# Performance work log

Hardware: AMD Instinct MI355X
Metric: run time of the kernel (lower is better)

Reference implementation:

```python
import jax, jax.numpy as jnp
import numpy as np

B, T, D, L = 16, 4096, 512, 1024

def setup_inputs() -> dict:
    key = jax.random.key(0)
    k1, k2, k3, k4 = jax.random.split(key, 4)
    x = jax.random.normal(k1, (B, T, D), dtype=jnp.float32)
    q = jax.random.normal(k2, (L, D), dtype=jnp.float32)
    fc_w = jax.random.normal(k3, (1, D), dtype=jnp.float32) * (1.0 / np.sqrt(D))
    fc_b = jax.random.normal(k4, (1,), dtype=jnp.float32) * 0.01
    return {"x": x, "q": q, "fc_w": fc_w, "fc_b": fc_b}

def reference(x, q, fc_w, fc_b):
    # att: (B, T, L) label-wise attention scores, softmax over sequence axis T
    att = jnp.einsum('btd,ld->btl', x, q)
    att = jax.nn.softmax(att, axis=1)
    # out: (B, L, D) attention-pooled features per label
    out = jnp.einsum('btl,btd->bld', att, x)
    # linear head to scalar per label -> (B, L)
    return jnp.einsum('bld,od->blo', out, fc_w).squeeze(-1) + fc_b[0]
```

## Files before the change

### kernel.cpp

```cpp
#include <hip/hip_runtime.h>

#define B_ 16
#define T_ 4096
#define D_ 512
#define L_ 1024
#define NTCH (T_ / 64)
#define PPLANE ((size_t)B_ * NTCH * L_)

typedef _Float16 half8 __attribute__((ext_vector_type(8)));
typedef float float4v __attribute__((ext_vector_type(4)));

__device__ inline void gl_lds(const void* g, void* l) {
    __builtin_amdgcn_global_load_lds(
        (const __attribute__((address_space(1))) unsigned int*)g,
        (__attribute__((address_space(3))) unsigned int*)l, 16, 0, 0);
}

__global__ __launch_bounds__(256) void k_prep(const float* __restrict__ src,
                                              const float* __restrict__ w,
                                              _Float16* __restrict__ dst,
                                              float* __restrict__ y, int do_y) {
    __shared__ float Yp[64];
    const int tid  = threadIdx.x;
    const int wv   = tid >> 6;
    const int lane = tid & 63;
    const int row  = lane & 15, gq = lane >> 4;
    const float* bsrc = src + (size_t)blockIdx.x * (16 * 512);
    half8* bdst = (half8*)dst + (size_t)blockIdx.x * 1024;

    float acc = 0.f;
#pragma unroll
    for (int it = 0; it < 4; ++it) {
        int kc = it * 4 + wv;
        int k0 = kc * 32 + gq * 8;
        float4 a = *(const float4*)(bsrc + row * 512 + k0);
        float4 c = *(const float4*)(bsrc + row * 512 + k0 + 4);
        half8 h;
        h[0] = (_Float16)a.x; h[1] = (_Float16)a.y; h[2] = (_Float16)a.z; h[3] = (_Float16)a.w;
        h[4] = (_Float16)c.x; h[5] = (_Float16)c.y; h[6] = (_Float16)c.z; h[7] = (_Float16)c.w;
        bdst[kc * 64 + lane] = h;
        if (do_y) {
            float4 wa = *(const float4*)(w + k0);
            float4 wc = *(const float4*)(w + k0 + 4);
            acc = fmaf(a.x, wa.x, acc); acc = fmaf(a.y, wa.y, acc);
            acc = fmaf(a.z, wa.z, acc); acc = fmaf(a.w, wa.w, acc);
            acc = fmaf(c.x, wc.x, acc); acc = fmaf(c.y, wc.y, acc);
            acc = fmaf(c.z, wc.z, acc); acc = fmaf(c.w, wc.w, acc);
        }
    }
    if (do_y) {
        acc += __shfl_xor(acc, 16, 64);
        acc += __shfl_xor(acc, 32, 64);
        if (gq == 0) Yp[wv * 16 + row] = acc;
        __syncthreads();
        if (tid < 16)
            y[blockIdx.x * 16 + tid] = Yp[tid] + Yp[16 + tid] + Yp[32 + tid] + Yp[48 + tid];
    }
}

__global__ __launch_bounds__(256, 4) void k_mfma(const _Float16* __restrict__ xt,
                                                 const _Float16* __restrict__ qt,
                                                 const float* __restrict__ y,
                                                 float* __restrict__ part) {
    __shared__ half8 S[1024];
    __shared__ float ys[128];

    const int bid  = blockIdx.x;
    const int xcd  = bid & 7;
    const int jj   = bid >> 3;
    const int tile = (xcd << 6) | (jj >> 3);
    const int lblk = jj & 7;
    const int tblk = tile & 31;
    const int b    = tile >> 5;

    const int tid  = threadIdx.x;
    const int lane = tid & 63;
    const int w    = tid >> 6;
    const int tb0  = b * (T_ / 16) + tblk * 8;
    const int lb0  = lblk * 8;

    if (tid < 128) ys[tid] = y[(size_t)b * T_ + tblk * 128 + tid];

    float4v acc[4][4];
#pragma unroll
    for (int i = 0; i < 4; ++i)
#pragma unroll
        for (int j = 0; j < 4; ++j) acc[i][j] = (float4v){0.f, 0.f, 0.f, 0.f};

    const half8* Xg = (const half8*)xt;
    const half8* Qg = (const half8*)qt;
    const int xa = tb0 + 2 * w;
    const int qa = lb0 + 2 * w;
    const int ts = (w >> 1) * 4, ls = (w & 1) * 4;

    for (int kc = 0; kc < D_ / 32; ++kc) {
        __syncthreads();
        gl_lds(Xg + ((size_t)xa * (D_ / 32) + kc) * 64 + lane,       &S[(2 * w) * 64]);
        gl_lds(Xg + ((size_t)(xa + 1) * (D_ / 32) + kc) * 64 + lane, &S[(2 * w + 1) * 64]);
        gl_lds(Qg + ((size_t)qa * (D_ / 32) + kc) * 64 + lane,       &S[512 + (2 * w) * 64]);
        gl_lds(Qg + ((size_t)(qa + 1) * (D_ / 32) + kc) * 64 + lane, &S[512 + (2 * w + 1) * 64]);
        __syncthreads();

        half8 A[4], Bv[4];
#pragma unroll
        for (int i = 0; i < 4; ++i) A[i] = S[(ts + i) * 64 + lane];
#pragma unroll
        for (int j = 0; j < 4; ++j) Bv[j] = S[512 + (ls + j) * 64 + lane];
#pragma unroll
        for (int i = 0; i < 4; ++i)
#pragma unroll
            for (int j = 0; j < 4; ++j)
                acc[i][j] = __builtin_amdgcn_mfma_f32_16x16x32_f16(A[i], Bv[j], acc[i][j], 0, 0, 0);
    }

    const int quad = lane >> 4, cl = lane & 15;
    const int tw = (w >> 1) * 64;
    const int tchunk = tblk * 2 + (w >> 1);
    const int lbase = lblk * 128 + (w & 1) * 64;

    float* pm = part;
    float* pz = part + PPLANE;
    float* pn = part + 2 * PPLANE;

#pragma unroll
    for (int j = 0; j < 4; ++j) {
        float m = -1e30f;
#pragma unroll
        for (int i = 0; i < 4; ++i)
#pragma unroll
            for (int r = 0; r < 4; ++r) m = fmaxf(m, acc[i][j][r]);
        float z = 0.f, n = 0.f;
#pragma unroll
        for (int i = 0; i < 4; ++i)
#pragma unroll
            for (int r = 0; r < 4; ++r) {
                float p = __expf(acc[i][j][r] - m);
                z += p;
                n = fmaf(p, ys[tw + i * 16 + quad * 4 + r], n);
            }
#pragma unroll
        for (int msk = 16; msk <= 32; msk <<= 1) {
            float om = __shfl_xor(m, msk, 64);
            float oz = __shfl_xor(z, msk, 64);
            float on = __shfl_xor(n, msk, 64);
            float mn = fmaxf(m, om);
            float s0 = __expf(m - mn), s1 = __expf(om - mn);
            z = fmaf(z, s0, oz * s1);
            n = fmaf(n, s0, on * s1);
            m = mn;
        }
        if (quad == 0) {
            int l = lbase + j * 16 + cl;
            size_t a = ((size_t)b * NTCH + tchunk) * L_ + l;
            pm[a] = m;
            pz[a] = z;
            pn[a] = n;
        }
    }
}

__global__ __launch_bounds__(256) void k_comb_p(const float* __restrict__ part,
                                                const float* __restrict__ fc_b,
                                                float* __restrict__ out) {
    int bl = blockIdx.x * 256 + threadIdx.x;
    int b = bl >> 10, l = bl & (L_ - 1);
    const float* pm = part;
    const float* pz = part + PPLANE;
    const float* pn = part + 2 * PPLANE;
    float m = -1e30f, z = 0.f, n = 0.f;
    for (int c = 0; c < NTCH; ++c) {
        size_t a = ((size_t)b * NTCH + c) * L_ + l;
        float pmv = pm[a], pzv = pz[a], pnv = pn[a];
        float mn = fmaxf(m, pmv);
        float s0 = __expf(m - mn), s1 = __expf(pmv - mn);
        z = fmaf(z, s0, pzv * s1);
        n = fmaf(n, s0, pnv * s1);
        m = mn;
    }
    out[bl] = n / z + fc_b[0];
}

#define NC 8
#define TC (T_ / NC)
#define BT 128
#define BL 128
#define KK 32

__global__ __launch_bounds__(256) void k_y(const float* __restrict__ x,
                                           const float* __restrict__ w,
                                           float* __restrict__ y) {
    int row  = (blockIdx.x * 256 + threadIdx.x) >> 6;
    int lane = threadIdx.x & 63;
    const float* r = x + (size_t)row * D_;
    float s = 0.f;
#pragma unroll
    for (int k = 0; k < D_; k += 64) s = fmaf(r[k + lane], w[k + lane], s);
#pragma unroll
    for (int o = 32; o > 0; o >>= 1) s += __shfl_xor(s, o, 64);
    if (lane == 0) y[row] = s;
}

__global__ __launch_bounds__(256, 2) void k_main(const float* __restrict__ x,
                                                 const float* __restrict__ q,
                                                 const float* __restrict__ y,
                                                 float* __restrict__ part) {
    __shared__ float Xs[KK][BT + 4];
    __shared__ float Qs[KK][BL + 4];
    const int tid = threadIdx.x;
    const int ty = tid & 15, tx = tid >> 4;
    const int lb = blockIdx.x * BL, chunk = blockIdx.y, b = blockIdx.z;
    const int g = tid & 7, r0 = tid >> 3;

    float run_m[8], run_z[8], run_n[8];
#pragma unroll
    for (int j = 0; j < 8; ++j) { run_m[j] = -1e30f; run_z[j] = 0.f; run_n[j] = 0.f; }

    for (int tt = 0; tt < TC; tt += BT) {
        const int t0 = chunk * TC + tt;
        float s[8][8];
#pragma unroll
        for (int i = 0; i < 8; ++i)
#pragma unroll
            for (int j = 0; j < 8; ++j) s[i][j] = 0.f;
        for (int kc = 0; kc < D_; kc += KK) {
            __syncthreads();
#pragma unroll
            for (int p = 0; p < 4; ++p) {
                int rr = p * 32 + r0;
                float4 vx = *(const float4*)(x + ((size_t)b * T_ + t0 + rr) * D_ + kc + g * 4);
                float4 vq = *(const float4*)(q + (size_t)(lb + rr) * D_ + kc + g * 4);
                Xs[g * 4 + 0][rr] = vx.x; Xs[g * 4 + 1][rr] = vx.y;
                Xs[g * 4 + 2][rr] = vx.z; Xs[g * 4 + 3][rr] = vx.w;
                Qs[g * 4 + 0][rr] = vq.x; Qs[g * 4 + 1][rr] = vq.y;
                Qs[g * 4 + 2][rr] = vq.z; Qs[g * 4 + 3][rr] = vq.w;
            }
            __syncthreads();
#pragma unroll
            for (int k = 0; k < KK; ++k) {
                float4 a0 = *(const float4*)&Xs[k][ty * 4];
                float4 a1 = *(const float4*)&Xs[k][64 + ty * 4];
                float4 b0 = *(const float4*)&Qs[k][tx * 4];
                float4 b1 = *(const float4*)&Qs[k][64 + tx * 4];
                float av[8] = {a0.x, a0.y, a0.z, a0.w, a1.x, a1.y, a1.z, a1.w};
                float bv[8] = {b0.x, b0.y, b0.z, b0.w, b1.x, b1.y, b1.z, b1.w};
#pragma unroll
                for (int i = 0; i < 8; ++i)
#pragma unroll
                    for (int j = 0; j < 8; ++j) s[i][j] = fmaf(av[i], bv[j], s[i][j]);
            }
        }
        float yv[8];
#pragma unroll
        for (int i = 0; i < 8; ++i) {
            int tl = (i < 4) ? (ty * 4 + i) : (64 + ty * 4 + (i - 4));
            yv[i] = y[(size_t)b * T_ + t0 + tl];
        }
#pragma unroll
        for (int j = 0; j < 8; ++j) {
            float mt = s[0][j];
#pragma unroll
            for (int i = 1; i < 8; ++i) mt = fmaxf(mt, s[i][j]);
            float mn = fmaxf(run_m[j], mt);
            float sc = __expf(run_m[j] - mn);
            float z = run_z[j] * sc, n = run_n[j] * sc;
#pragma unroll
            for (int i = 0; i < 8; ++i) {
                float p = __expf(s[i][j] - mn);
                z += p;
                n = fmaf(p, yv[i], n);
            }
            run_m[j] = mn; run_z[j] = z; run_n[j] = n;
        }
    }
#pragma unroll
    for (int msk = 1; msk < 16; msk <<= 1) {
#pragma unroll
        for (int j = 0; j < 8; ++j) {
            float om = __shfl_xor(run_m[j], msk, 64);
            float oz = __shfl_xor(run_z[j], msk, 64);
            float on = __shfl_xor(run_n[j], msk, 64);
            float mn = fmaxf(run_m[j], om);
            float s0 = __expf(run_m[j] - mn), s1 = __expf(om - mn);
            run_z[j] = fmaf(run_z[j], s0, oz * s1);
            run_n[j] = fmaf(run_n[j], s0, on * s1);
            run_m[j] = mn;
        }
    }
    if (ty == 0) {
#pragma unroll
        for (int j = 0; j < 8; ++j) {
            int ll = (j < 4) ? (tx * 4 + j) : (64 + tx * 4 + (j - 4));
            size_t idx = ((size_t)(b * L_ + lb + ll) * NC + chunk) * 3;
            part[idx + 0] = run_m[j];
            part[idx + 1] = run_z[j];
            part[idx + 2] = run_n[j];
        }
    }
}

__global__ __launch_bounds__(256) void k_comb_f(const float* __restrict__ part,
                                                const float* __restrict__ fc_b,
                                                float* __restrict__ out) {
    int bl = blockIdx.x * 256 + threadIdx.x;
    float m = -1e30f, z = 0.f, n = 0.f;
    for (int c = 0; c < NC; ++c) {
        size_t idx = ((size_t)bl * NC + c) * 3;
        float pm = part[idx + 0], pz = part[idx + 1], pn = part[idx + 2];
        float mn = fmaxf(m, pm);
        float s0 = __expf(m - mn), s1 = __expf(pm - mn);
        z = fmaf(z, s0, pz * s1);
        n = fmaf(n, s0, pn * s1);
        m = mn;
    }
    out[bl] = n / z + fc_b[0];
}

extern "C" void kernel_launch(void* const* d_in, const int* in_sizes, int n_in,
                              void* d_out, int out_size, void* d_ws, size_t ws_size,
                              hipStream_t stream) {
    const float* x    = (const float*)d_in[0];
    const float* q    = (const float*)d_in[1];
    const float* fc_w = (const float*)d_in[2];
    const float* fc_b = (const float*)d_in[3];
    float* out = (float*)d_out;
    float* ws  = (float*)d_ws;

    const size_t Y_F    = (size_t)B_ * T_;
    const size_t PART_F = 3 * PPLANE;
    const size_t XT_H   = (size_t)B_ * T_ * D_;
    const size_t QT_H   = (size_t)L_ * D_;
    const size_t need   = (Y_F + PART_F) * 4 + (XT_H + QT_H) * 2;

    if (ws_size >= need) {
        float* y    = ws;
        float* part = ws + Y_F;
        _Float16* xt = (_Float16*)(ws + Y_F + PART_F);
        _Float16* qt = xt + XT_H;
        k_prep<<<B_ * T_ / 16, 256, 0, stream>>>(x, fc_w, xt, y, 1);
        k_prep<<<L_ / 16, 256, 0, stream>>>(q, fc_w, qt, nullptr, 0);
        k_mfma<<<4096, 256, 0, stream>>>(xt, qt, y, part);
        k_comb_p<<<B_ * L_ / 256, 256, 0, stream>>>(part, fc_b, out);
    } else {
        float* y    = ws;
        float* part = ws + Y_F;
        k_y   <<<B_ * T_ / 4, 256, 0, stream>>>(x, fc_w, y);
        k_main<<<dim3(L_ / BL, NC, B_), 256, 0, stream>>>(x, q, y, part);
        k_comb_f<<<B_ * L_ / 256, 256, 0, stream>>>(part, fc_b, out);
    }
}
```

Baseline: 290.6 us.

## Stage prep rows through LDS, merge prep launches, double K-step per sync in MFMA

The prep kernel now loads each 16x512 fp32 tile with fully coalesced float4 reads into padded shared memory before converting to fp16. The separate x and q prep launches are merged into one grid, saving a launch. The MFMA kernel loads two 32-wide K chunks per barrier pair, halving the number of synchronisations at the cost of doubling LDS use per block to 32KB. That may lower occupancy at the requested 4 blocks per SM.

```diff
diff --git a/kernel.cpp b/kernel.cpp
--- a/kernel.cpp
+++ b/kernel.cpp
@@ -6,6 +6,7 @@
 #define L_ 1024
 #define NTCH (T_ / 64)
 #define PPLANE ((size_t)B_ * NTCH * L_)
+#define XBLK (B_ * T_ / 16)
 
 typedef _Float16 half8 __attribute__((ext_vector_type(8)));
 typedef float float4v __attribute__((ext_vector_type(4)));
@@ -16,30 +17,42 @@
         (__attribute__((address_space(3))) unsigned int*)l, 16, 0, 0);
 }
 
-__global__ __launch_bounds__(256) void k_prep(const float* __restrict__ src,
+__global__ __launch_bounds__(256) void k_prep(const float* __restrict__ x,
+                                              const float* __restrict__ q,
                                               const float* __restrict__ w,
-                                              _Float16* __restrict__ dst,
-                                              float* __restrict__ y, int do_y) {
+                                              _Float16* __restrict__ xt,
+                                              _Float16* __restrict__ qt,
+                                              float* __restrict__ y) {
+    __shared__ float Xl[16 * 516];
     __shared__ float Yp[64];
-    const int tid  = threadIdx.x;
-    const int wv   = tid >> 6;
-    const int lane = tid & 63;
-    const int row  = lane & 15, gq = lane >> 4;
-    const float* bsrc = src + (size_t)blockIdx.x * (16 * 512);
-    half8* bdst = (half8*)dst + (size_t)blockIdx.x * 1024;
-
+    const int tid = threadIdx.x;
+    const bool isq = blockIdx.x >= XBLK;
+    const int blk = isq ? (blockIdx.x - XBLK) : blockIdx.x;
+    const float* bsrc = (isq ? q : x) + (size_t)blk * (16 * 512);
+    half8* dst = (half8*)(isq ? qt : xt) + (size_t)blk * 1024;
+
+#pragma unroll
+    for (int it = 0; it < 8; ++it) {
+        int f = it * 1024 + tid * 4;
+        int row = f >> 9, k = f & 511;
+        *(float4*)&Xl[row * 516 + k] = *(const float4*)(bsrc + f);
+    }
+    __syncthreads();
+
+    const int wv = tid >> 6, lane = tid & 63;
+    const int row = lane & 15, gq = lane >> 4;
     float acc = 0.f;
 #pragma unroll
     for (int it = 0; it < 4; ++it) {
         int kc = it * 4 + wv;
         int k0 = kc * 32 + gq * 8;
-        float4 a = *(const float4*)(bsrc + row * 512 + k0);
-        float4 c = *(const float4*)(bsrc + row * 512 + k0 + 4);
+        float4 a = *(const float4*)&Xl[row * 516 + k0];
+        float4 c = *(const float4*)&Xl[row * 516 + k0 + 4];
         half8 h;
         h[0] = (_Float16)a.x; h[1] = (_Float16)a.y; h[2] = (_Float16)a.z; h[3] = (_Float16)a.w;
         h[4] = (_Float16)c.x; h[5] = (_Float16)c.y; h[6] = (_Float16)c.z; h[7] = (_Float16)c.w;
-        bdst[kc * 64 + lane] = h;
-        if (do_y) {
+        dst[kc * 64 + lane] = h;
+        if (!isq) {
             float4 wa = *(const float4*)(w + k0);
             float4 wc = *(const float4*)(w + k0 + 4);
             acc = fmaf(a.x, wa.x, acc); acc = fmaf(a.y, wa.y, acc);
@@ -48,13 +61,13 @@
             acc = fmaf(c.z, wc.z, acc); acc = fmaf(c.w, wc.w, acc);
         }
     }
-    if (do_y) {
+    if (!isq) {
         acc += __shfl_xor(acc, 16, 64);
         acc += __shfl_xor(acc, 32, 64);
         if (gq == 0) Yp[wv * 16 + row] = acc;
         __syncthreads();
         if (tid < 16)
-            y[blockIdx.x * 16 + tid] = Yp[tid] + Yp[16 + tid] + Yp[32 + tid] + Yp[48 + tid];
+            y[blk * 16 + tid] = Yp[tid] + Yp[16 + tid] + Yp[32 + tid] + Yp[48 + tid];
     }
 }
 
@@ -62,7 +75,7 @@
                                                  const _Float16* __restrict__ qt,
                                                  const float* __restrict__ y,
                                                  float* __restrict__ part) {
-    __shared__ half8 S[1024];
+    __shared__ half8 S[2048];
     __shared__ float ys[128];
 
     const int bid  = blockIdx.x;
@@ -93,24 +106,35 @@
     const int qa = lb0 + 2 * w;
     const int ts = (w >> 1) * 4, ls = (w & 1) * 4;
 
-    for (int kc = 0; kc < D_ / 32; ++kc) {
+    for (int kk = 0; kk < D_ / 64; ++kk) {
+        const int kc0 = kk * 2;
         __syncthreads();
-        gl_lds(Xg + ((size_t)xa * (D_ / 32) + kc) * 64 + lane,       &S[(2 * w) * 64]);
-        gl_lds(Xg + ((size_t)(xa + 1) * (D_ / 32) + kc) * 64 + lane, &S[(2 * w + 1) * 64]);
-        gl_lds(Qg + ((size_t)qa * (D_ / 32) + kc) * 64 + lane,       &S[512 + (2 * w) * 64]);
-        gl_lds(Qg + ((size_t)(qa + 1) * (D_ / 32) + kc) * 64 + lane, &S[512 + (2 * w + 1) * 64]);
+#pragma unroll
+        for (int s = 0; s < 2; ++s) {
+            gl_lds(Xg + ((size_t)xa * (D_ / 32) + kc0 + s) * 64 + lane,
+                   &S[s * 512 + (2 * w) * 64]);
+            gl_lds(Xg + ((size_t)(xa + 1) * (D_ / 32) + kc0 + s) * 64 + lane,
+                   &S[s * 512 + (2 * w + 1) * 64]);
+            gl_lds(Qg + ((size_t)qa * (D_ / 32) + kc0 + s) * 64 + lane,
+                   &S[1024 + s * 512 + (2 * w) * 64]);
+            gl_lds(Qg + ((size_t)(qa + 1) * (D_ / 32) + kc0 + s) * 64 + lane,
+                   &S[1024 + s * 512 + (2 * w + 1) * 64]);
+        }
         __syncthreads();
 
-        half8 A[4], Bv[4];
-#pragma unroll
-        for (int i = 0; i < 4; ++i) A[i] = S[(ts + i) * 64 + lane];
-#pragma unroll
-        for (int j = 0; j < 4; ++j) Bv[j] = S[512 + (ls + j) * 64 + lane];
-#pragma unroll
-        for (int i = 0; i < 4; ++i)
-#pragma unroll
-            for (int j = 0; j < 4; ++j)
-                acc[i][j] = __builtin_amdgcn_mfma_f32_16x16x32_f16(A[i], Bv[j], acc[i][j], 0, 0, 0);
+#pragma unroll
+        for (int s = 0; s < 2; ++s) {
+            half8 A[4], Bv[4];
+#pragma unroll
+            for (int i = 0; i < 4; ++i) A[i] = S[s * 512 + (ts + i) * 64 + lane];
+#pragma unroll
+            for (int j = 0; j < 4; ++j) Bv[j] = S[1024 + s * 512 + (ls + j) * 64 + lane];
+#pragma unroll
+            for (int i = 0; i < 4; ++i)
+#pragma unroll
+                for (int j = 0; j < 4; ++j)
+                    acc[i][j] = __builtin_amdgcn_mfma_f32_16x16x32_f16(A[i], Bv[j], acc[i][j], 0, 0, 0);
+        }
     }
 
     const int quad = lane >> 4, cl = lane & 15;
@@ -336,8 +360,7 @@
         float* part = ws + Y_F;
         _Float16* xt = (_Float16*)(ws + Y_F + PART_F);
         _Float16* qt = xt + XT_H;
-        k_prep<<<B_ * T_ / 16, 256, 0, stream>>>(x, fc_w, xt, y, 1);
-        k_prep<<<L_ / 16, 256, 0, stream>>>(q, fc_w, qt, nullptr, 0);
+        k_prep<<<XBLK + L_ / 16, 256, 0, stream>>>(x, q, fc_w, xt, qt, y);
         k_mfma<<<4096, 256, 0, stream>>>(xt, qt, y, part);
         k_comb_p<<<B_ * L_ / 256, 256, 0, stream>>>(part, fc_b, out);
     } else {
```

Result: faster. 282.0 us (-3.0%).
